# Kernel tuning notes

Hardware: AMD Instinct MI355X
Metric: run time of the kernel (lower is better)

The kernel has to match this reference:

```python
import jax, jax.numpy as jnp
import numpy as np

B, T, N = 32, 24, 512
DIM_IN, DIM_OUT, HID, EMB = 64, 2, 128, 16
NEG_SLOPE = 0.01  # nn.LeakyReLU default


def leaky_relu(x):
    return jnp.where(x >= 0, x, NEG_SLOPE * x)


def setup_inputs() -> dict:
    key = jax.random.key(0)
    ks = jax.random.split(key, 11)
    return {
        "eb": jax.random.normal(ks[0], (B, T, N, DIM_IN), jnp.float32),
        "time_eb": jax.random.normal(ks[1], (B, T, EMB), jnp.float32),
        "node_eb": jax.random.normal(ks[2], (N, EMB), jnp.float32),
        # ln1: Linear(dim_in, hidden) stored as [dim_in, hidden] (x @ W + b)
        "W1": jax.random.normal(ks[3], (DIM_IN, HID), jnp.float32) / np.sqrt(DIM_IN),
        "b1": jax.random.normal(ks[4], (HID,), jnp.float32) * 0.01,
        # ln3: Linear(hidden, dim_out)
        "W3": jax.random.normal(ks[5], (HID, DIM_OUT), jnp.float32) / np.sqrt(HID),
        "b3": jax.random.normal(ks[6], (DIM_OUT,), jnp.float32) * 0.01,
        "weights_pool_spa": jax.random.normal(ks[7], (EMB, HID, HID), jnp.float32),
        "bias_pool_spa": jax.random.normal(ks[8], (EMB, HID), jnp.float32),
        "weights_pool_tem": jax.random.normal(ks[9], (EMB, HID, HID), jnp.float32),
        "bias_pool_tem": jax.random.normal(ks[10], (EMB, HID), jnp.float32),
    }


def reference(eb, time_eb, node_eb, W1, b1, W3, b3,
              weights_pool_spa, bias_pool_spa,
              weights_pool_tem, bias_pool_tem):
    # eb: [b,t,n,dim_in] -> [b,t,n,hidden]
    eb_out = eb @ W1 + b1
    # spatial hypernetwork: per-node weight [n,hid,hid] and bias [n,hid]
    weights_spa = jnp.einsum('nd,dio->nio', node_eb, weights_pool_spa)
    bias_spa = node_eb @ bias_pool_spa  # [n,hid]
    out_spa = leaky_relu(jnp.einsum('btni,nio->btno', eb_out, weights_spa) + bias_spa)
    # temporal hypernetwork: per-(b,t) weight [b,t,hid,hid] and bias [b,t,1,hid]
    weights_tem = jnp.einsum('btd,dio->btio', time_eb, weights_pool_tem)
    bias_tem = (time_eb @ bias_pool_tem)[:, :, None, :]
    out_tem = leaky_relu(jnp.einsum('btni,btio->btno', out_spa, weights_tem) + bias_tem)
    logits = out_tem @ W3 + b3  # [b,t,n,dim_out]
    return logits
```

## Files before the change

### kernel.cpp

```cpp
#include <hip/hip_runtime.h>
#include <hip/hip_bf16.h>
#include <stdint.h>

#define BT   768
#define NN   512
#define DIN  64
#define HID  128
#define EMB  16
#define SLOPE 0.01f

typedef __attribute__((ext_vector_type(8))) short bf16x8;
typedef __attribute__((ext_vector_type(4))) float f32x4;
typedef __attribute__((ext_vector_type(4))) short short4v;

__device__ __forceinline__ short f2bf(float f) {
    uint32_t u = __float_as_uint(f);
    u += 0x7fff + ((u >> 16) & 1);
    return (short)(u >> 16);
}
__device__ __forceinline__ float bf2f(short s) {
    return __uint_as_float(((uint32_t)(unsigned short)s) << 16);
}

static const size_t OFF_WCOMB = 0;
static const size_t OFF_WTEM  = 8388608;
static const size_t OFF_BSPA  = 33554432;
static const size_t OFF_BTEM  = 33816576;
static const size_t OFF_Q     = 34209792;
static const size_t OFF_PTT   = 34217984;
static const size_t OFF_PTS2  = 34742272;
static const size_t OFF_H2    = 35004416;

__global__ __launch_bounds__(256)
void k_prep(const float* __restrict__ pool_spa, const float* __restrict__ pool_tem,
            const float* __restrict__ W1, const float* __restrict__ b1,
            const float* __restrict__ bp_spa, const float* __restrict__ bp_tem,
            const float* __restrict__ node_eb, const float* __restrict__ time_eb,
            short* __restrict__ ptt, short* __restrict__ pts2,
            float* __restrict__ qtab, float* __restrict__ bspa,
            float* __restrict__ btem)
{
    const int b = blockIdx.x, t = threadIdx.x;
    __shared__ short smem[26112];

    if (b < 64) {
        const int d = b >> 2, o0 = (b & 3) * 32;
        short* s = smem;
        #pragma unroll
        for (int c = 0; c < 16; ++c) {
            int e = c * 256 + t;
            int i = e >> 5, oo = e & 31;
            s[oo * 136 + i] = f2bf(pool_tem[(d * HID + i) * HID + o0 + oo]);
        }
        __syncthreads();
        #pragma unroll
        for (int c = 0; c < 8; ++c) {
            int e = c * 256 + t;
            int oo = e >> 6, ii = (e & 63) * 2;
            uint32_t lo = (unsigned short)s[oo * 136 + ii];
            uint32_t hi = (unsigned short)s[oo * 136 + ii + 1];
            ((uint32_t*)ptt)[((d * HID + o0 + oo) * HID + ii) >> 1] = lo | (hi << 16);
        }
        return;
    }
    if (b < 224) {
        int q = (b - 64) * 256 + t;
        const float *bp, *emb; float* outp;
        if (q < NN * 32) { bp = bp_spa; emb = node_eb; outp = bspa; }
        else { q -= NN * 32; bp = bp_tem; emb = time_eb; outp = btem; }
        const int n = q >> 5, oq = q & 31;
        float4 a = make_float4(0.f, 0.f, 0.f, 0.f);
        #pragma unroll
        for (int d = 0; d < EMB; ++d) {
            float e = emb[n * EMB + d];
            float4 bv = ((const float4*)bp)[d * 32 + oq];
            a.x += e * bv.x; a.y += e * bv.y; a.z += e * bv.z; a.w += e * bv.w;
        }
        ((float4*)outp)[q] = a;
        return;
    }
    if (b < 226) {
        const int dbase = (b - 224) * 8;
        if (t < 128) {
            float a[8] = {};
            for (int i = 0; i < HID; ++i) {
                float bv = b1[i];
                #pragma unroll
                for (int dd = 0; dd < 8; ++dd)
                    a[dd] += bv * pool_spa[((dbase + dd) * HID + i) * HID + t];
            }
            #pragma unroll
            for (int dd = 0; dd < 8; ++dd) qtab[(dbase + dd) * HID + t] = a[dd];
        }
        return;
    }
    {
        const int d = b - 226;
        const int wave = t >> 6, lane = t & 63, quad = lane >> 4, l15 = lane & 15;
        const int m0 = wave * 32;
        short* sPT  = smem;
        short* sW1b = smem + 128 * 136;
        #pragma unroll
        for (int c = 0; c < 64; ++c) {
            int idx = c * 256 + t;
            int i = idx >> 7, o = idx & 127;
            sPT[o * 136 + i] = f2bf(pool_spa[(d * HID + i) * HID + o]);
        }
        #pragma unroll
        for (int c = 0; c < 32; ++c) {
            int idx = c * 256 + t;
            sW1b[(idx >> 7) * 136 + (idx & 127)] = f2bf(W1[idx]);
        }
        __syncthreads();
        f32x4 acc[2][4] = {};
        #pragma unroll
        for (int kc = 0; kc < 4; ++kc) {
            bf16x8 a0 = *(const bf16x8*)(sPT + (m0 + l15) * 136 + kc * 32 + quad * 8);
            bf16x8 a1 = *(const bf16x8*)(sPT + (m0 + 16 + l15) * 136 + kc * 32 + quad * 8);
            #pragma unroll
            for (int tc = 0; tc < 4; ++tc) {
                bf16x8 bb = *(const bf16x8*)(sW1b + (tc * 16 + l15) * 136 + kc * 32 + quad * 8);
                acc[0][tc] = __builtin_amdgcn_mfma_f32_16x16x32_bf16(a0, bb, acc[0][tc], 0, 0, 0);
                acc[1][tc] = __builtin_amdgcn_mfma_f32_16x16x32_bf16(a1, bb, acc[1][tc], 0, 0, 0);
            }
        }
        __syncthreads();
        short* sO = smem;
        #pragma unroll
        for (int tr = 0; tr < 2; ++tr)
            #pragma unroll
            for (int tc = 0; tc < 4; ++tc)
                #pragma unroll
                for (int r = 0; r < 4; ++r)
                    sO[(m0 + tr * 16 + quad * 4 + r) * 72 + tc * 16 + l15] = f2bf(acc[tr][tc][r]);
        __syncthreads();
        #pragma unroll
        for (int c = 0; c < 4; ++c) {
            int idx = c * 256 + t;
            int row = idx >> 3, ko = (idx & 7) * 8;
            *(bf16x8*)(pts2 + (size_t)d * 8192 + row * 64 + ko) =
                *(const bf16x8*)(sO + row * 72 + ko);
        }
    }
}

__global__ __launch_bounds__(256)
void k_genw(const short* __restrict__ pts2, const short* __restrict__ ptt,
            const float* __restrict__ node_eb, const float* __restrict__ time_eb,
            short* __restrict__ wcomb, short* __restrict__ wtem)
{
    const int t = threadIdx.x, b = blockIdx.x;
    int nb, cq, stride;
    const short* pool; const float* emb; short* outp;
    if (b < 64) {
        nb = b >> 3; cq = (b & 7) * 256 + t; stride = 2048;
        pool = pts2; emb = node_eb; outp = wcomb;
    } else {
        int bb = b - 64;
        nb = bb >> 4; cq = (bb & 15) * 256 + t; stride = 4096;
        pool = ptt; emb = time_eb; outp = wtem;
    }
    __shared__ float sEmb[64 * EMB];
    #pragma unroll
    for (int c = 0; c < 4; ++c) {
        int idx = c * 256 + t;
        sEmb[idx] = emb[nb * 64 * EMB + idx];
    }
    __syncthreads();
    float4 p[EMB];
    #pragma unroll
    for (int d = 0; d < EMB; ++d) {
        short4v v = ((const short4v*)pool)[d * stride + cq];
        p[d] = make_float4(bf2f(v.x), bf2f(v.y), bf2f(v.z), bf2f(v.w));
    }
    for (int nn = 0; nn < 64; ++nn) {
        float4 a = make_float4(0.f, 0.f, 0.f, 0.f);
        #pragma unroll
        for (int d = 0; d < EMB; ++d) {
            float e = sEmb[nn * EMB + d];
            a.x += e * p[d].x; a.y += e * p[d].y;
            a.z += e * p[d].z; a.w += e * p[d].w;
        }
        short4v o;
        o.x = f2bf(a.x); o.y = f2bf(a.y); o.z = f2bf(a.z); o.w = f2bf(a.w);
        ((short4v*)outp)[(size_t)(nb * 64 + nn) * stride + cq] = o;
    }
}

__global__ __launch_bounds__(256)
void k_spatial(const float* __restrict__ eb, const short* __restrict__ wcomb,
               const float* __restrict__ bspa, const float* __restrict__ qtab,
               const float* __restrict__ node_eb, short* __restrict__ h2)
{
    const int n = blockIdx.x;
    const int t = threadIdx.x;
    const int wave = t >> 6, lane = t & 63, quad = lane >> 4, l15 = lane & 15;
    const int m0 = (wave >> 1) * 32, n0 = (wave & 1) * 64;

    __shared__ short sW[128 * 72];
    __shared__ short sEb[2][64 * 72];
    __shared__ short sOut[2][64 * 136];

    const float* ebn = eb + (size_t)n * DIN;
    short* h2n = h2 + (size_t)n * (BT * HID);

    bf16x8 wreg[4];
    {
        const bf16x8* src = (const bf16x8*)(wcomb + (size_t)n * 8192);
        #pragma unroll
        for (int c = 0; c < 4; ++c) wreg[c] = src[c * 256 + t];
    }
    float4 ev[4];
    #pragma unroll
    for (int c = 0; c < 4; ++c) {
        int idx = c * 256 + t;
        int r = idx >> 4, kq = (idx & 15) * 4;
        ev[c] = *(const float4*)(ebn + (size_t)r * (NN * DIN) + kq);
    }
    float bsr[4];
    #pragma unroll
    for (int tc = 0; tc < 4; ++tc) {
        int col = n0 + tc * 16 + l15;
        float a = bspa[n * HID + col];
        #pragma unroll
        for (int d = 0; d < EMB; ++d)
            a += node_eb[n * EMB + d] * qtab[d * HID + col];
        bsr[tc] = a;
    }
    #pragma unroll
    for (int c = 0; c < 4; ++c) {
        int idx = c * 256 + t;
        *(bf16x8*)(sW + (idx >> 3) * 72 + (idx & 7) * 8) = wreg[c];
    }
    #pragma unroll
    for (int c = 0; c < 4; ++c) {
        int idx = c * 256 + t;
        int r = idx >> 4, kq = (idx & 15) * 4;
        short4v s;
        s.x = f2bf(ev[c].x); s.y = f2bf(ev[c].y);
        s.z = f2bf(ev[c].z); s.w = f2bf(ev[c].w);
        *(short4v*)(sEb[0] + r * 72 + kq) = s;
    }
    __syncthreads();

    for (int ch = 0; ch < 12; ++ch) {
        const int cur = ch & 1, nxt = cur ^ 1;
        if (ch < 11) {
            #pragma unroll
            for (int c = 0; c < 4; ++c) {
                int idx = c * 256 + t;
                int r = (ch + 1) * 64 + (idx >> 4), kq = (idx & 15) * 4;
                ev[c] = *(const float4*)(ebn + (size_t)r * (NN * DIN) + kq);
            }
        }
        f32x4 acc[2][4] = {};
        #pragma unroll
        for (int kc = 0; kc < 2; ++kc) {
            bf16x8 a0 = *(const bf16x8*)(sEb[cur] + (m0 + l15) * 72 + kc * 32 + quad * 8);
            bf16x8 a1 = *(const bf16x8*)(sEb[cur] + (m0 + 16 + l15) * 72 + kc * 32 + quad * 8);
            #pragma unroll
            for (int tc = 0; tc < 4; ++tc) {
                bf16x8 bfr = *(const bf16x8*)(sW + (n0 + tc * 16 + l15) * 72 + kc * 32 + quad * 8);
                acc[0][tc] = __builtin_amdgcn_mfma_f32_16x16x32_bf16(a0, bfr, acc[0][tc], 0, 0, 0);
                acc[1][tc] = __builtin_amdgcn_mfma_f32_16x16x32_bf16(a1, bfr, acc[1][tc], 0, 0, 0);
            }
        }
        #pragma unroll
        for (int tr = 0; tr < 2; ++tr)
            #pragma unroll
            for (int tc = 0; tc < 4; ++tc) {
                int col = n0 + tc * 16 + l15;
                #pragma unroll
                for (int r = 0; r < 4; ++r) {
                    float v = acc[tr][tc][r] + bsr[tc];
                    v = (v >= 0.f) ? v : SLOPE * v;
                    sOut[cur][(m0 + tr * 16 + quad * 4 + r) * 136 + col] = f2bf(v);
                }
            }
        if (ch < 11) {
            #pragma unroll
            for (int c = 0; c < 4; ++c) {
                int idx = c * 256 + t;
                int r = idx >> 4, kq = (idx & 15) * 4;
                short4v s;
                s.x = f2bf(ev[c].x); s.y = f2bf(ev[c].y);
                s.z = f2bf(ev[c].z); s.w = f2bf(ev[c].w);
                *(short4v*)(sEb[nxt] + r * 72 + kq) = s;
            }
        }
        __syncthreads();
        #pragma unroll
        for (int c = 0; c < 4; ++c) {
            int idx = c * 256 + t;
            *(bf16x8*)(h2n + (size_t)ch * (64 * HID) + (size_t)idx * 8) =
                *(const bf16x8*)(sOut[cur] + (idx >> 4) * 136 + (idx & 15) * 8);
        }
    }
}

__global__ __launch_bounds__(256)
void k_temporal(const short* __restrict__ h2, const short* __restrict__ wtem,
                const float* __restrict__ btem, const float* __restrict__ W3,
                const float* __restrict__ b3, float* __restrict__ out)
{
    const int R = blockIdx.x, nbase = blockIdx.y * 256;
    const int t = threadIdx.x;
    const int wave = t >> 6, lane = t & 63, quad = lane >> 4, l15 = lane & 15;
    const int m0 = wave * 16;

    __shared__ short sWt[128 * 136];
    __shared__ short sH2[64 * 136];

    const short* hb = h2 + (size_t)R * HID;

    bf16x8 wv[8];
    {
        const bf16x8* src = (const bf16x8*)(wtem + (size_t)R * 16384);
        #pragma unroll
        for (int c = 0; c < 8; ++c) wv[c] = src[c * 256 + t];
    }
    bf16x8 hreg[4];
    #pragma unroll
    for (int c = 0; c < 4; ++c) {
        int idx = c * 256 + t;
        hreg[c] = *(const bf16x8*)(hb + (size_t)(nbase + (idx >> 4)) * (BT * HID) + (idx & 15) * 8);
    }
    float btr[8], w3r0[8], w3r1[8];
    #pragma unroll
    for (int tc = 0; tc < 8; ++tc) {
        int o = tc * 16 + l15;
        btr[tc] = btem[R * HID + o];
        w3r0[tc] = W3[2 * o]; w3r1[tc] = W3[2 * o + 1];
    }
    const float b30 = b3[0], b31 = b3[1];

    #pragma unroll
    for (int c = 0; c < 8; ++c) {
        int idx = c * 256 + t;
        *(bf16x8*)(sWt + (idx >> 4) * 136 + (idx & 15) * 8) = wv[c];
    }
    #pragma unroll
    for (int c = 0; c < 4; ++c) {
        int idx = c * 256 + t;
        *(bf16x8*)(sH2 + (idx >> 4) * 136 + (idx & 15) * 8) = hreg[c];
    }
    __syncthreads();

    for (int nt = 0; nt < 4; ++nt) {
        if (nt < 3) {
            #pragma unroll
            for (int c = 0; c < 4; ++c) {
                int idx = c * 256 + t;
                hreg[c] = *(const bf16x8*)(hb + (size_t)(nbase + (nt + 1) * 64 + (idx >> 4)) * (BT * HID) + (idx & 15) * 8);
            }
        }
        f32x4 acc[8] = {};
        #pragma unroll
        for (int kc = 0; kc < 4; ++kc) {
            bf16x8 a = *(const bf16x8*)(sH2 + (m0 + l15) * 136 + kc * 32 + quad * 8);
            #pragma unroll
            for (int tc = 0; tc < 8; ++tc) {
                bf16x8 b = *(const bf16x8*)(sWt + (tc * 16 + l15) * 136 + kc * 32 + quad * 8);
                acc[tc] = __builtin_amdgcn_mfma_f32_16x16x32_bf16(a, b, acc[tc], 0, 0, 0);
            }
        }
        float pl[4][2] = {};
        #pragma unroll
        for (int tc = 0; tc < 8; ++tc) {
            #pragma unroll
            for (int r = 0; r < 4; ++r) {
                float v = acc[tc][r] + btr[tc];
                v = (v >= 0.f) ? v : SLOPE * v;
                pl[r][0] += v * w3r0[tc];
                pl[r][1] += v * w3r1[tc];
            }
        }
        #pragma unroll
        for (int m = 1; m <= 8; m <<= 1)
            #pragma unroll
            for (int r = 0; r < 4; ++r) {
                pl[r][0] += __shfl_xor(pl[r][0], m);
                pl[r][1] += __shfl_xor(pl[r][1], m);
            }
        if (l15 == 0) {
            #pragma unroll
            for (int r = 0; r < 4; ++r) {
                int nrow = nbase + nt * 64 + m0 + quad * 4 + r;
                *(float2*)(out + ((size_t)R * NN + nrow) * 2) =
                    make_float2(pl[r][0] + b30, pl[r][1] + b31);
            }
        }
        __syncthreads();
        if (nt < 3) {
            #pragma unroll
            for (int c = 0; c < 4; ++c) {
                int idx = c * 256 + t;
                *(bf16x8*)(sH2 + (idx >> 4) * 136 + (idx & 15) * 8) = hreg[c];
            }
            __syncthreads();
        }
    }
}

extern "C" void kernel_launch(void* const* d_in, const int* in_sizes, int n_in,
                              void* d_out, int out_size, void* d_ws, size_t ws_size,
                              hipStream_t stream) {
    const float* eb        = (const float*)d_in[0];
    const float* time_eb   = (const float*)d_in[1];
    const float* node_eb   = (const float*)d_in[2];
    const float* W1        = (const float*)d_in[3];
    const float* b1        = (const float*)d_in[4];
    const float* W3        = (const float*)d_in[5];
    const float* b3        = (const float*)d_in[6];
    const float* pool_spa  = (const float*)d_in[7];
    const float* bpool_spa = (const float*)d_in[8];
    const float* pool_tem  = (const float*)d_in[9];
    const float* bpool_tem = (const float*)d_in[10];
    float* out = (float*)d_out;

    char* ws = (char*)d_ws;
    short* wcomb = (short*)(ws + OFF_WCOMB);
    short* wtem  = (short*)(ws + OFF_WTEM);
    float* bspa  = (float*)(ws + OFF_BSPA);
    float* btem  = (float*)(ws + OFF_BTEM);
    float* qtab  = (float*)(ws + OFF_Q);
    short* ptt   = (short*)(ws + OFF_PTT);
    short* pts2  = (short*)(ws + OFF_PTS2);
    short* h2    = (short*)(ws + OFF_H2);

    k_prep<<<242, 256, 0, stream>>>(pool_spa, pool_tem, W1, b1, bpool_spa, bpool_tem,
                                    node_eb, time_eb, ptt, pts2, qtab, bspa, btem);
    k_genw<<<256, 256, 0, stream>>>(pts2, ptt, node_eb, time_eb, wcomb, wtem);
    k_spatial<<<dim3(NN), 256, 0, stream>>>(eb, wcomb, bspa, qtab, node_eb, h2);
    k_temporal<<<dim3(BT, 2), 256, 0, stream>>>(h2, wtem, btem, W3, b3, out);
}
```

Baseline: 252.0 us.

## Process four nodes per spatial block with per-wave register-resident weights

The spatial kernel now gives each block four adjacent nodes and one quarter of the BT rows, with each wave owning one node. Each eb row read is 256 contiguous floats across the four nodes instead of 64 floats per node, so global loads coalesce better. The per-node weight fragments stay in registers instead of being reloaded from shared memory. This raises register pressure (16 bf16x8 B fragments plus 16 accumulators), and each wave writes its own h2 output slice without a block-wide barrier before the store.

Result: slower. 257.5 us (+2.2%).

```diff
diff --git a/kernel.cpp b/kernel.cpp
--- a/kernel.cpp
+++ b/kernel.cpp
@@ -187,40 +187,39 @@
     }
 }
 
+#define NSL 2320
 __global__ __launch_bounds__(256)
 void k_spatial(const float* __restrict__ eb, const short* __restrict__ wcomb,
                const float* __restrict__ bspa, const float* __restrict__ qtab,
                const float* __restrict__ node_eb, short* __restrict__ h2)
 {
-    const int n = blockIdx.x;
+    const int n0 = blockIdx.x * 4;
+    const int Rbase = blockIdx.y * 192;
     const int t = threadIdx.x;
     const int wave = t >> 6, lane = t & 63, quad = lane >> 4, l15 = lane & 15;
-    const int m0 = (wave >> 1) * 32, n0 = (wave & 1) * 64;
-
-    __shared__ short sW[128 * 72];
-    __shared__ short sEb[2][64 * 72];
-    __shared__ short sOut[2][64 * 136];
-
-    const float* ebn = eb + (size_t)n * DIN;
-    short* h2n = h2 + (size_t)n * (BT * HID);
-
-    bf16x8 wreg[4];
-    {
-        const bf16x8* src = (const bf16x8*)(wcomb + (size_t)n * 8192);
-        #pragma unroll
-        for (int c = 0; c < 4; ++c) wreg[c] = src[c * 256 + t];
-    }
-    float4 ev[4];
-    #pragma unroll
-    for (int c = 0; c < 4; ++c) {
-        int idx = c * 256 + t;
-        int r = idx >> 4, kq = (idx & 15) * 4;
-        ev[c] = *(const float4*)(ebn + (size_t)r * (NN * DIN) + kq);
-    }
-    float bsr[4];
-    #pragma unroll
-    for (int tc = 0; tc < 4; ++tc) {
-        int col = n0 + tc * 16 + l15;
+    const int n = n0 + wave;
+
+    __shared__ short sEb[2][4 * NSL];
+    __shared__ short sOut[4][32 * 136];
+
+    float4 ev[8];
+    #pragma unroll
+    for (int c = 0; c < 8; ++c) {
+        int idx = c * 256 + t;
+        int r = idx >> 6, f4 = idx & 63;
+        ev[c] = *(const float4*)(eb + (size_t)(Rbase + r) * (NN * DIN) + n0 * DIN + f4 * 4);
+    }
+    bf16x8 Breg[8][2];
+    #pragma unroll
+    for (int tc = 0; tc < 8; ++tc)
+        #pragma unroll
+        for (int kc = 0; kc < 2; ++kc)
+            Breg[tc][kc] = *(const bf16x8*)(wcomb + (size_t)n * 8192
+                                            + (tc * 16 + l15) * 64 + kc * 32 + quad * 8);
+    float bsr[8];
+    #pragma unroll
+    for (int tc = 0; tc < 8; ++tc) {
+        int col = tc * 16 + l15;
         float a = bspa[n * HID + col];
         #pragma unroll
         for (int d = 0; d < EMB; ++d)
@@ -228,73 +227,73 @@
         bsr[tc] = a;
     }
     #pragma unroll
-    for (int c = 0; c < 4; ++c) {
-        int idx = c * 256 + t;
-        *(bf16x8*)(sW + (idx >> 3) * 72 + (idx & 7) * 8) = wreg[c];
-    }
-    #pragma unroll
-    for (int c = 0; c < 4; ++c) {
-        int idx = c * 256 + t;
-        int r = idx >> 4, kq = (idx & 15) * 4;
+    for (int c = 0; c < 8; ++c) {
+        int idx = c * 256 + t;
+        int r = idx >> 6, nsl = (idx & 63) >> 4, k4 = (idx & 15) * 4;
         short4v s;
         s.x = f2bf(ev[c].x); s.y = f2bf(ev[c].y);
         s.z = f2bf(ev[c].z); s.w = f2bf(ev[c].w);
-        *(short4v*)(sEb[0] + r * 72 + kq) = s;
+        *(short4v*)(&sEb[0][nsl * NSL + r * 72 + k4]) = s;
     }
     __syncthreads();
 
-    for (int ch = 0; ch < 12; ++ch) {
-        const int cur = ch & 1, nxt = cur ^ 1;
-        if (ch < 11) {
-            #pragma unroll
-            for (int c = 0; c < 4; ++c) {
+    short* h2w = h2 + (size_t)n * (BT * HID) + (size_t)Rbase * HID;
+    short* so  = &sOut[wave][0];
+
+    int cur = 0;
+    for (int ch = 0; ch < 6; ++ch) {
+        if (ch < 5) {
+            #pragma unroll
+            for (int c = 0; c < 8; ++c) {
                 int idx = c * 256 + t;
-                int r = (ch + 1) * 64 + (idx >> 4), kq = (idx & 15) * 4;
-                ev[c] = *(const float4*)(ebn + (size_t)r * (NN * DIN) + kq);
-            }
-        }
-        f32x4 acc[2][4] = {};
+                int r = (ch + 1) * 32 + (idx >> 6), f4 = idx & 63;
+                ev[c] = *(const float4*)(eb + (size_t)(Rbase + r) * (NN * DIN) + n0 * DIN + f4 * 4);
+            }
+        }
+        const short* se = &sEb[cur][wave * NSL];
+        f32x4 acc[2][8] = {};
         #pragma unroll
         for (int kc = 0; kc < 2; ++kc) {
-            bf16x8 a0 = *(const bf16x8*)(sEb[cur] + (m0 + l15) * 72 + kc * 32 + quad * 8);
-            bf16x8 a1 = *(const bf16x8*)(sEb[cur] + (m0 + 16 + l15) * 72 + kc * 32 + quad * 8);
-            #pragma unroll
-            for (int tc = 0; tc < 4; ++tc) {
-                bf16x8 bfr = *(const bf16x8*)(sW + (n0 + tc * 16 + l15) * 72 + kc * 32 + quad * 8);
-                acc[0][tc] = __builtin_amdgcn_mfma_f32_16x16x32_bf16(a0, bfr, acc[0][tc], 0, 0, 0);
-                acc[1][tc] = __builtin_amdgcn_mfma_f32_16x16x32_bf16(a1, bfr, acc[1][tc], 0, 0, 0);
+            bf16x8 a0 = *(const bf16x8*)(se + l15 * 72 + kc * 32 + quad * 8);
+            bf16x8 a1 = *(const bf16x8*)(se + (16 + l15) * 72 + kc * 32 + quad * 8);
+            #pragma unroll
+            for (int tc = 0; tc < 8; ++tc) {
+                acc[0][tc] = __builtin_amdgcn_mfma_f32_16x16x32_bf16(a0, Breg[tc][kc], acc[0][tc], 0, 0, 0);
+                acc[1][tc] = __builtin_amdgcn_mfma_f32_16x16x32_bf16(a1, Breg[tc][kc], acc[1][tc], 0, 0, 0);
             }
         }
         #pragma unroll
         for (int tr = 0; tr < 2; ++tr)
             #pragma unroll
-            for (int tc = 0; tc < 4; ++tc) {
-                int col = n0 + tc * 16 + l15;
+            for (int tc = 0; tc < 8; ++tc) {
+                int col = tc * 16 + l15;
                 #pragma unroll
                 for (int r = 0; r < 4; ++r) {
                     float v = acc[tr][tc][r] + bsr[tc];
                     v = (v >= 0.f) ? v : SLOPE * v;
-                    sOut[cur][(m0 + tr * 16 + quad * 4 + r) * 136 + col] = f2bf(v);
+                    so[(tr * 16 + quad * 4 + r) * 136 + col] = f2bf(v);
                 }
             }
-        if (ch < 11) {
-            #pragma unroll
-            for (int c = 0; c < 4; ++c) {
+        if (ch < 5) {
+            #pragma unroll
+            for (int c = 0; c < 8; ++c) {
                 int idx = c * 256 + t;
-                int r = idx >> 4, kq = (idx & 15) * 4;
+                int r = idx >> 6, nsl = (idx & 63) >> 4, k4 = (idx & 15) * 4;
                 short4v s;
                 s.x = f2bf(ev[c].x); s.y = f2bf(ev[c].y);
                 s.z = f2bf(ev[c].z); s.w = f2bf(ev[c].w);
-                *(short4v*)(sEb[nxt] + r * 72 + kq) = s;
-            }
-        }
-        __syncthreads();
-        #pragma unroll
-        for (int c = 0; c < 4; ++c) {
-            int idx = c * 256 + t;
-            *(bf16x8*)(h2n + (size_t)ch * (64 * HID) + (size_t)idx * 8) =
-                *(const bf16x8*)(sOut[cur] + (idx >> 4) * 136 + (idx & 15) * 8);
-        }
+                *(short4v*)(&sEb[cur ^ 1][nsl * NSL + r * 72 + k4]) = s;
+            }
+            __syncthreads();
+        }
+        #pragma unroll
+        for (int c = 0; c < 8; ++c) {
+            int idx = c * 64 + lane;
+            int row = idx >> 4, colg = (idx & 15) * 8;
+            *(bf16x8*)(h2w + (size_t)(ch * 32 + row) * HID + colg) =
+                *(const bf16x8*)(so + row * 136 + colg);
+        }
+        cur ^= 1;
     }
 }
 
@@ -431,6 +430,6 @@
     k_prep<<<242, 256, 0, stream>>>(pool_spa, pool_tem, W1, b1, bpool_spa, bpool_tem,
                                     node_eb, time_eb, ptt, pts2, qtab, bspa, btem);
     k_genw<<<256, 256, 0, stream>>>(pts2, ptt, node_eb, time_eb, wcomb, wtem);
-    k_spatial<<<dim3(NN), 256, 0, stream>>>(eb, wcomb, bspa, qtab, node_eb, h2);
+    k_spatial<<<dim3(128, 4), 256, 0, stream>>>(eb, wcomb, bspa, qtab, node_eb, h2);
     k_temporal<<<dim3(BT, 2), 256, 0, stream>>>(h2, wtem, btem, W3, b3, out);
 }
```

## Fuse hypernetwork weight generation into spatial and temporal kernels

Applied to the files above, without the earlier changes.

Removes the k_genw kernel and the materialized per-node and per-(b,t) weight tensors. Each spatial and temporal block now builds its own weight matrix in shared memory from the bf16 pools and the embedding row. The separate bias precompute is also dropped: the spatial bias is folded into the q table, and the temporal bias is computed inline. This cuts one launch and tens of MB of workspace writes and reads, at the cost of redundant per-block embedding-combination FMAs. The temporal grid is changed so one block covers all 512 nodes, with launch bounds set for 3 blocks per CU.

Result: faster. 243.1 us (-3.5%).

```diff
diff --git a/kernel.cpp b/kernel.cpp
--- a/kernel.cpp
+++ b/kernel.cpp
@@ -22,23 +22,17 @@
     return __uint_as_float(((uint32_t)(unsigned short)s) << 16);
 }
 
-static const size_t OFF_WCOMB = 0;
-static const size_t OFF_WTEM  = 8388608;
-static const size_t OFF_BSPA  = 33554432;
-static const size_t OFF_BTEM  = 33816576;
-static const size_t OFF_Q     = 34209792;
-static const size_t OFF_PTT   = 34217984;
-static const size_t OFF_PTS2  = 34742272;
-static const size_t OFF_H2    = 35004416;
+static const size_t OFF_PTT  = 0;
+static const size_t OFF_PTS2 = 524288;
+static const size_t OFF_QB   = 786432;
+static const size_t OFF_H2   = 1048576;
 
 __global__ __launch_bounds__(256)
 void k_prep(const float* __restrict__ pool_spa, const float* __restrict__ pool_tem,
             const float* __restrict__ W1, const float* __restrict__ b1,
-            const float* __restrict__ bp_spa, const float* __restrict__ bp_tem,
-            const float* __restrict__ node_eb, const float* __restrict__ time_eb,
+            const float* __restrict__ bp_spa,
             short* __restrict__ ptt, short* __restrict__ pts2,
-            float* __restrict__ qtab, float* __restrict__ bspa,
-            float* __restrict__ btem)
+            float* __restrict__ qb)
 {
     const int b = blockIdx.x, t = threadIdx.x;
     __shared__ short smem[26112];
@@ -63,26 +57,12 @@
         }
         return;
     }
-    if (b < 224) {
-        int q = (b - 64) * 256 + t;
-        const float *bp, *emb; float* outp;
-        if (q < NN * 32) { bp = bp_spa; emb = node_eb; outp = bspa; }
-        else { q -= NN * 32; bp = bp_tem; emb = time_eb; outp = btem; }
-        const int n = q >> 5, oq = q & 31;
-        float4 a = make_float4(0.f, 0.f, 0.f, 0.f);
-        #pragma unroll
-        for (int d = 0; d < EMB; ++d) {
-            float e = emb[n * EMB + d];
-            float4 bv = ((const float4*)bp)[d * 32 + oq];
-            a.x += e * bv.x; a.y += e * bv.y; a.z += e * bv.z; a.w += e * bv.w;
-        }
-        ((float4*)outp)[q] = a;
-        return;
-    }
-    if (b < 226) {
-        const int dbase = (b - 224) * 8;
+    if (b < 66) {
+        const int dbase = (b - 64) * 8;
         if (t < 128) {
-            float a[8] = {};
+            float a[8];
+            #pragma unroll
+            for (int dd = 0; dd < 8; ++dd) a[dd] = bp_spa[(dbase + dd) * HID + t];
             for (int i = 0; i < HID; ++i) {
                 float bv = b1[i];
                 #pragma unroll
@@ -90,12 +70,12 @@
                     a[dd] += bv * pool_spa[((dbase + dd) * HID + i) * HID + t];
             }
             #pragma unroll
-            for (int dd = 0; dd < 8; ++dd) qtab[(dbase + dd) * HID + t] = a[dd];
+            for (int dd = 0; dd < 8; ++dd) qb[(dbase + dd) * HID + t] = a[dd];
         }
         return;
     }
     {
-        const int d = b - 226;
+        const int d = b - 66;
         const int wave = t >> 6, lane = t & 63, quad = lane >> 4, l15 = lane & 15;
         const int m0 = wave * 32;
         short* sPT  = smem;
@@ -145,52 +125,9 @@
 }
 
 __global__ __launch_bounds__(256)
-void k_genw(const short* __restrict__ pts2, const short* __restrict__ ptt,
-            const float* __restrict__ node_eb, const float* __restrict__ time_eb,
-            short* __restrict__ wcomb, short* __restrict__ wtem)
-{
-    const int t = threadIdx.x, b = blockIdx.x;
-    int nb, cq, stride;
-    const short* pool; const float* emb; short* outp;
-    if (b < 64) {
-        nb = b >> 3; cq = (b & 7) * 256 + t; stride = 2048;
-        pool = pts2; emb = node_eb; outp = wcomb;
-    } else {
-        int bb = b - 64;
-        nb = bb >> 4; cq = (bb & 15) * 256 + t; stride = 4096;
-        pool = ptt; emb = time_eb; outp = wtem;
-    }
-    __shared__ float sEmb[64 * EMB];
-    #pragma unroll
-    for (int c = 0; c < 4; ++c) {
-        int idx = c * 256 + t;
-        sEmb[idx] = emb[nb * 64 * EMB + idx];
-    }
-    __syncthreads();
-    float4 p[EMB];
-    #pragma unroll
-    for (int d = 0; d < EMB; ++d) {
-        short4v v = ((const short4v*)pool)[d * stride + cq];
-        p[d] = make_float4(bf2f(v.x), bf2f(v.y), bf2f(v.z), bf2f(v.w));
-    }
-    for (int nn = 0; nn < 64; ++nn) {
-        float4 a = make_float4(0.f, 0.f, 0.f, 0.f);
-        #pragma unroll
-        for (int d = 0; d < EMB; ++d) {
-            float e = sEmb[nn * EMB + d];
-            a.x += e * p[d].x; a.y += e * p[d].y;
-            a.z += e * p[d].z; a.w += e * p[d].w;
-        }
-        short4v o;
-        o.x = f2bf(a.x); o.y = f2bf(a.y); o.z = f2bf(a.z); o.w = f2bf(a.w);
-        ((short4v*)outp)[(size_t)(nb * 64 + nn) * stride + cq] = o;
-    }
-}
-
-__global__ __launch_bounds__(256)
-void k_spatial(const float* __restrict__ eb, const short* __restrict__ wcomb,
-               const float* __restrict__ bspa, const float* __restrict__ qtab,
-               const float* __restrict__ node_eb, short* __restrict__ h2)
+void k_spatial(const float* __restrict__ eb, const short* __restrict__ pts2,
+               const float* __restrict__ qb, const float* __restrict__ node_eb,
+               short* __restrict__ h2)
 {
     const int n = blockIdx.x;
     const int t = threadIdx.x;
@@ -204,12 +141,6 @@
     const float* ebn = eb + (size_t)n * DIN;
     short* h2n = h2 + (size_t)n * (BT * HID);
 
-    bf16x8 wreg[4];
-    {
-        const bf16x8* src = (const bf16x8*)(wcomb + (size_t)n * 8192);
-        #pragma unroll
-        for (int c = 0; c < 4; ++c) wreg[c] = src[c * 256 + t];
-    }
     float4 ev[4];
     #pragma unroll
     for (int c = 0; c < 4; ++c) {
@@ -217,20 +148,33 @@
         int r = idx >> 4, kq = (idx & 15) * 4;
         ev[c] = *(const float4*)(ebn + (size_t)r * (NN * DIN) + kq);
     }
+    float ne[EMB];
+    #pragma unroll
+    for (int d = 0; d < EMB; ++d) ne[d] = node_eb[n * EMB + d];
     float bsr[4];
     #pragma unroll
     for (int tc = 0; tc < 4; ++tc) {
         int col = n0 + tc * 16 + l15;
-        float a = bspa[n * HID + col];
-        #pragma unroll
-        for (int d = 0; d < EMB; ++d)
-            a += node_eb[n * EMB + d] * qtab[d * HID + col];
+        float a = 0.f;
+        #pragma unroll
+        for (int d = 0; d < EMB; ++d) a += ne[d] * qb[d * HID + col];
         bsr[tc] = a;
     }
     #pragma unroll
     for (int c = 0; c < 4; ++c) {
         int idx = c * 256 + t;
-        *(bf16x8*)(sW + (idx >> 3) * 72 + (idx & 7) * 8) = wreg[c];
+        int o = idx >> 3, k0 = (idx & 7) * 8;
+        float a8[8] = {};
+        #pragma unroll
+        for (int d = 0; d < EMB; ++d) {
+            bf16x8 pv = *(const bf16x8*)(pts2 + (size_t)d * 8192 + o * 64 + k0);
+            #pragma unroll
+            for (int e = 0; e < 8; ++e) a8[e] += ne[d] * bf2f(pv[e]);
+        }
+        bf16x8 w;
+        #pragma unroll
+        for (int e = 0; e < 8; ++e) w[e] = f2bf(a8[e]);
+        *(bf16x8*)(sW + o * 72 + k0) = w;
     }
     #pragma unroll
     for (int c = 0; c < 4; ++c) {
@@ -298,12 +242,13 @@
     }
 }
 
-__global__ __launch_bounds__(256)
-void k_temporal(const short* __restrict__ h2, const short* __restrict__ wtem,
-                const float* __restrict__ btem, const float* __restrict__ W3,
-                const float* __restrict__ b3, float* __restrict__ out)
+__global__ __launch_bounds__(256, 3)
+void k_temporal(const short* __restrict__ h2, const short* __restrict__ ptt,
+                const float* __restrict__ bp_tem, const float* __restrict__ time_eb,
+                const float* __restrict__ W3, const float* __restrict__ b3,
+                float* __restrict__ out)
 {
-    const int R = blockIdx.x, nbase = blockIdx.y * 256;
+    const int R = blockIdx.x;
     const int t = threadIdx.x;
     const int wave = t >> 6, lane = t & 63, quad = lane >> 4, l15 = lane & 15;
     const int m0 = wave * 16;
@@ -313,45 +258,56 @@
 
     const short* hb = h2 + (size_t)R * HID;
 
-    bf16x8 wv[8];
-    {
-        const bf16x8* src = (const bf16x8*)(wtem + (size_t)R * 16384);
-        #pragma unroll
-        for (int c = 0; c < 8; ++c) wv[c] = src[c * 256 + t];
-    }
     bf16x8 hreg[4];
     #pragma unroll
     for (int c = 0; c < 4; ++c) {
         int idx = c * 256 + t;
-        hreg[c] = *(const bf16x8*)(hb + (size_t)(nbase + (idx >> 4)) * (BT * HID) + (idx & 15) * 8);
+        hreg[c] = *(const bf16x8*)(hb + (size_t)(idx >> 4) * (BT * HID) + (idx & 15) * 8);
+    }
+    float te[EMB];
+    #pragma unroll
+    for (int d = 0; d < EMB; ++d) te[d] = time_eb[R * EMB + d];
+    #pragma unroll
+    for (int c = 0; c < 8; ++c) {
+        int idx = c * 256 + t;
+        int o = idx >> 4, i0 = (idx & 15) * 8;
+        float a8[8] = {};
+        #pragma unroll
+        for (int d = 0; d < EMB; ++d) {
+            bf16x8 pv = *(const bf16x8*)(ptt + (size_t)d * 16384 + o * 128 + i0);
+            #pragma unroll
+            for (int e = 0; e < 8; ++e) a8[e] += te[d] * bf2f(pv[e]);
+        }
+        bf16x8 w;
+        #pragma unroll
+        for (int e = 0; e < 8; ++e) w[e] = f2bf(a8[e]);
+        *(bf16x8*)(sWt + o * 136 + i0) = w;
     }
     float btr[8], w3r0[8], w3r1[8];
     #pragma unroll
     for (int tc = 0; tc < 8; ++tc) {
         int o = tc * 16 + l15;
-        btr[tc] = btem[R * HID + o];
+        float a = 0.f;
+        #pragma unroll
+        for (int d = 0; d < EMB; ++d) a += te[d] * bp_tem[d * HID + o];
+        btr[tc] = a;
         w3r0[tc] = W3[2 * o]; w3r1[tc] = W3[2 * o + 1];
     }
     const float b30 = b3[0], b31 = b3[1];
 
     #pragma unroll
-    for (int c = 0; c < 8; ++c) {
-        int idx = c * 256 + t;
-        *(bf16x8*)(sWt + (idx >> 4) * 136 + (idx & 15) * 8) = wv[c];
-    }
-    #pragma unroll
     for (int c = 0; c < 4; ++c) {
         int idx = c * 256 + t;
         *(bf16x8*)(sH2 + (idx >> 4) * 136 + (idx & 15) * 8) = hreg[c];
     }
     __syncthreads();
 
-    for (int nt = 0; nt < 4; ++nt) {
-        if (nt < 3) {
+    for (int nt = 0; nt < 8; ++nt) {
+        if (nt < 7) {
             #pragma unroll
             for (int c = 0; c < 4; ++c) {
                 int idx = c * 256 + t;
-                hreg[c] = *(const bf16x8*)(hb + (size_t)(nbase + (nt + 1) * 64 + (idx >> 4)) * (BT * HID) + (idx & 15) * 8);
+                hreg[c] = *(const bf16x8*)(hb + (size_t)((nt + 1) * 64 + (idx >> 4)) * (BT * HID) + (idx & 15) * 8);
             }
         }
         f32x4 acc[8] = {};
@@ -385,13 +341,13 @@
         if (l15 == 0) {
             #pragma unroll
             for (int r = 0; r < 4; ++r) {
-                int nrow = nbase + nt * 64 + m0 + quad * 4 + r;
+                int nrow = nt * 64 + m0 + quad * 4 + r;
                 *(float2*)(out + ((size_t)R * NN + nrow) * 2) =
                     make_float2(pl[r][0] + b30, pl[r][1] + b31);
             }
         }
         __syncthreads();
-        if (nt < 3) {
+        if (nt < 7) {
             #pragma unroll
             for (int c = 0; c < 4; ++c) {
                 int idx = c * 256 + t;
@@ -419,18 +375,13 @@
     float* out = (float*)d_out;
 
     char* ws = (char*)d_ws;
-    short* wcomb = (short*)(ws + OFF_WCOMB);
-    short* wtem  = (short*)(ws + OFF_WTEM);
-    float* bspa  = (float*)(ws + OFF_BSPA);
-    float* btem  = (float*)(ws + OFF_BTEM);
-    float* qtab  = (float*)(ws + OFF_Q);
-    short* ptt   = (short*)(ws + OFF_PTT);
-    short* pts2  = (short*)(ws + OFF_PTS2);
-    short* h2    = (short*)(ws + OFF_H2);
-
-    k_prep<<<242, 256, 0, stream>>>(pool_spa, pool_tem, W1, b1, bpool_spa, bpool_tem,
-                                    node_eb, time_eb, ptt, pts2, qtab, bspa, btem);
-    k_genw<<<256, 256, 0, stream>>>(pts2, ptt, node_eb, time_eb, wcomb, wtem);
-    k_spatial<<<dim3(NN), 256, 0, stream>>>(eb, wcomb, bspa, qtab, node_eb, h2);
-    k_temporal<<<dim3(BT, 2), 256, 0, stream>>>(h2, wtem, btem, W3, b3, out);
-}
+    short* ptt  = (short*)(ws + OFF_PTT);
+    short* pts2 = (short*)(ws + OFF_PTS2);
+    float* qb   = (float*)(ws + OFF_QB);
+    short* h2   = (short*)(ws + OFF_H2);
+
+    k_prep<<<82, 256, 0, stream>>>(pool_spa, pool_tem, W1, b1, bpool_spa,
+                                   ptt, pts2, qb);
+    k_spatial<<<dim3(NN), 256, 0, stream>>>(eb, pts2, qb, node_eb, h2);
+    k_temporal<<<dim3(BT), 256, 0, stream>>>(h2, ptt, bpool_tem, time_eb, W3, b3, out);
+}
```
